# Kernel optimization log

Hardware: AMD Instinct MI355X
Metric: run time of the kernel (lower is better)

## Reference

```python
import jax, jax.numpy as jnp
import numpy as np

NUM_USERS = 100000
NUM_ITEMS = 50000
EMB_DIM = 64
N_LAYERS = 3
NUM_BICLIQUES = 20000
E_ADJ = 1200000
E_HV = 400000
E_HU = 400000


def setup_inputs() -> dict:
    key = jax.random.key(0)
    ks = jax.random.split(key, 11)
    N = NUM_USERS + NUM_ITEMS
    return {
        "user_emb": jax.random.normal(ks[0], (NUM_USERS, EMB_DIM), dtype=jnp.float32) * 0.1,
        "item_emb": jax.random.normal(ks[1], (NUM_ITEMS, EMB_DIM), dtype=jnp.float32) * 0.1,
        "adj_val": jax.random.uniform(ks[2], (E_ADJ,), dtype=jnp.float32),
        "hv_val": jax.random.uniform(ks[3], (E_HV,), dtype=jnp.float32),
        "hu_val": jax.random.uniform(ks[4], (E_HU,), dtype=jnp.float32),
        "adj_row": jax.random.randint(ks[5], (E_ADJ,), 0, N, dtype=jnp.int32),
        "adj_col": jax.random.randint(ks[6], (E_ADJ,), 0, N, dtype=jnp.int32),
        "hv_row": jax.random.randint(ks[7], (E_HV,), 0, NUM_BICLIQUES, dtype=jnp.int32),
        "hv_col": jax.random.randint(ks[8], (E_HV,), 0, NUM_ITEMS, dtype=jnp.int32),
        "hu_row": jax.random.randint(ks[9], (E_HU,), 0, NUM_USERS, dtype=jnp.int32),
        "hu_col": jax.random.randint(ks[10], (E_HU,), 0, NUM_BICLIQUES, dtype=jnp.int32),
    }


def _spmm(row, col, val, x, n_rows):
    # sparse [n_rows, n_cols] @ dense [n_cols, d] via gather + segment-sum
    return jax.ops.segment_sum(val[:, None] * x[col], row, num_segments=n_rows)


def _row_degree(row, val, n_rows):
    deg = jax.ops.segment_sum(val, row, num_segments=n_rows)
    return jnp.where(deg == 0, 1.0, deg)  # matches degree[degree == 0] = 1.0


def reference(user_emb, item_emb, adj_val, hv_val, hu_val,
              adj_row, adj_col, hv_row, hv_col, hu_row, hu_col):
    N = user_emb.shape[0] + item_emb.shape[0]
    # ---- LightGCN global encoder: mean over layer embeddings ----
    all_emb = jnp.concatenate([user_emb, item_emb], axis=0)  # [N, d]
    acc = all_emb
    e = all_emb
    for _ in range(N_LAYERS):
        e = _spmm(adj_row, adj_col, adj_val, e, N)
        acc = acc + e
    final = acc / (N_LAYERS + 1)
    u_global = final[: user_emb.shape[0]]
    i_global = final[user_emb.shape[0]:]
    # ---- Biclique local encoder ----
    biclique_feat = _spmm(hv_row, hv_col, hv_val, item_emb, NUM_BICLIQUES)  # [B, d]
    biclique_feat = biclique_feat / _row_degree(hv_row, hv_val, NUM_BICLIQUES)[:, None]
    u_local = _spmm(hu_row, hu_col, hu_val, biclique_feat, user_emb.shape[0])  # [U, d]
    u_local = u_local / _row_degree(hu_row, hu_val, user_emb.shape[0])[:, None]
    return (u_global + u_local, i_global)
```

## Files before the change

kernel.cpp:

```cpp
#include <hip/hip_runtime.h>

#define NUSERS 100000
#define NITEMS 50000
#define NTOT   150000
#define NBIC   20000
#define DIM    64

#define HV_BASE  NTOT
#define HU_BASE  (NTOT + NBIC)
#define NROWS_ALL (NTOT + NBIC + NUSERS)

#define ADJ_RPB  500
#define NB_ADJ   300
#define HV_RPB   200
#define NB_HV    100
#define HU_RPB   1000
#define NB_HU    100
#define NBKT     (NB_ADJ + NB_HV + NB_HU)
#define HSIZE    512

#define EDGE_CAP 5120
#define ROWS_CAP 1024
#define CHUNK    8192
#define PA_BLK   1024
#define PB_BLK   512

typedef _Float16 h8 __attribute__((ext_vector_type(8)));

__device__ __forceinline__ void bucket_of(int r, int& b, int& rl) {
    if (r < NTOT)          { int q = r / ADJ_RPB;               b = q;                rl = r - q * ADJ_RPB; }
    else if (r < HU_BASE)  { int rr = r - HV_BASE; int q = rr / HV_RPB;
                             b = NB_ADJ + q;                    rl = rr - q * HV_RPB; }
    else                   { int rr = r - HU_BASE; int q = rr / HU_RPB;
                             b = NB_ADJ + NB_HV + q;            rl = rr - q * HU_RPB; }
}

__global__ void to_half_kernel(const float* __restrict__ user,
                               const float* __restrict__ item,
                               _Float16* __restrict__ x16) {
    int i = blockIdx.x * blockDim.x + threadIdx.x;
    const int n8 = NTOT * DIM / 8;
    if (i >= n8) return;
    const int u8 = NUSERS * DIM / 8;
    const float4* src = (i < u8) ? (const float4*)user + 2 * (size_t)i
                                 : (const float4*)item + 2 * (size_t)(i - u8);
    float4 a = src[0], b = src[1];
    h8 h;
    h[0] = (_Float16)a.x; h[1] = (_Float16)a.y; h[2] = (_Float16)a.z; h[3] = (_Float16)a.w;
    h[4] = (_Float16)b.x; h[5] = (_Float16)b.y; h[6] = (_Float16)b.z; h[7] = (_Float16)b.w;
    ((h8*)x16)[i] = h;
}

__global__ void __launch_bounds__(PA_BLK)
phaseA_kernel(const int* __restrict__ adj_row, const int* __restrict__ adj_col,
              const float* __restrict__ adj_val,
              const int* __restrict__ hv_row, const int* __restrict__ hv_col,
              const float* __restrict__ hv_val,
              const int* __restrict__ hu_row, const int* __restrict__ hu_col,
              const float* __restrict__ hu_val,
              int* __restrict__ bkt_cnt, int2* __restrict__ tmp,
              int e_adj, int e_hv, int e_hu) {
    __shared__ int hist[HSIZE];
    __shared__ int lstart[HSIZE];
    __shared__ int destB[HSIZE];
    __shared__ int psum[HSIZE];
    __shared__ int2 stage[CHUNK];

    const int tid = threadIdx.x;
    const int e_all = e_adj + e_hv + e_hu;
    const int base = blockIdx.x * CHUNK;
    const int nloc = min(CHUNK, e_all - base);

    if (tid < HSIZE) hist[tid] = 0;
    __syncthreads();

    for (int i = tid; i < nloc; i += PA_BLK) {
        int t = base + i, r;
        if (t < e_adj)             r = adj_row[t];
        else if (t < e_adj + e_hv) r = HV_BASE + hv_row[t - e_adj];
        else                       r = HU_BASE + hu_row[t - e_adj - e_hv];
        int b, rl; bucket_of(r, b, rl);
        atomicAdd(&hist[b], 1);
    }
    __syncthreads();

    int v = 0;
    if (tid < HSIZE) { v = hist[tid]; psum[tid] = v; }
    __syncthreads();
    for (int off = 1; off < HSIZE; off <<= 1) {
        int t = 0;
        if (tid < HSIZE && tid >= off) t = psum[tid - off];
        __syncthreads();
        if (tid < HSIZE) psum[tid] += t;
        __syncthreads();
    }
    if (tid < HSIZE) lstart[tid] = psum[tid] - v;
    __syncthreads();

    if (tid < NBKT) {
        int c = hist[tid];
        if (c > 0)
            destB[tid] = tid * EDGE_CAP + atomicAdd(&bkt_cnt[tid], c) - lstart[tid];
    }
    __syncthreads();
    if (tid < HSIZE) hist[tid] = lstart[tid];
    __syncthreads();

    for (int i = tid; i < nloc; i += PA_BLK) {
        int t = base + i, r, c; float v2;
        if (t < e_adj)             { r = adj_row[t]; c = adj_col[t]; v2 = adj_val[t]; }
        else if (t < e_adj + e_hv) { int k = t - e_adj;
                                     r = HV_BASE + hv_row[k]; c = hv_col[k]; v2 = hv_val[k]; }
        else                       { int k = t - e_adj - e_hv;
                                     r = HU_BASE + hu_row[k]; c = hu_col[k]; v2 = hu_val[k]; }
        int b, rl; bucket_of(r, b, rl);
        int p = atomicAdd(&hist[b], 1);
        stage[p] = make_int2(c | (rl << 18), __float_as_int(v2));
    }
    __syncthreads();

    const int wave = tid >> 6, lane = tid & 63;
    for (int b = wave; b < NBKT; b += (PA_BLK / 64)) {
        int s = lstart[b];
        int e = hist[b];
        int d = destB[b];
        for (int j = s + lane; j < e; j += 64)
            tmp[d + j] = stage[j];
    }
}

__global__ void bkt_scan(const int* __restrict__ cnt, int* __restrict__ base) {
    __shared__ int s[HSIZE];
    int tid = threadIdx.x;
    int v = (tid < NBKT) ? cnt[tid] : 0;
    s[tid] = v;
    __syncthreads();
    for (int off = 1; off < HSIZE; off <<= 1) {
        int t = (tid >= off) ? s[tid - off] : 0;
        __syncthreads();
        s[tid] += t;
        __syncthreads();
    }
    if (tid < NBKT) base[tid] = s[tid] - v;
}

__global__ void __launch_bounds__(PB_BLK)
phaseB_kernel(const int* __restrict__ bkt_cnt, const int* __restrict__ bkt_base,
              const int2* __restrict__ tmp, int2* __restrict__ edges,
              int* __restrict__ start, int* __restrict__ cntArr) {
    __shared__ int  rh[ROWS_CAP];
    __shared__ int  rs[ROWS_CAP];
    __shared__ int  psum[PB_BLK];
    __shared__ int2 stage[EDGE_CAP];

    const int tid = threadIdx.x;
    const int b = blockIdx.x;
    int rlo, nR;
    if (b < NB_ADJ)              { rlo = b * ADJ_RPB;                          nR = ADJ_RPB; }
    else if (b < NB_ADJ + NB_HV) { rlo = HV_BASE + (b - NB_ADJ) * HV_RPB;      nR = HV_RPB; }
    else                         { rlo = HU_BASE + (b - NB_ADJ - NB_HV) * HU_RPB; nR = HU_RPB; }

    const int nE = bkt_cnt[b];
    const int gbase = bkt_base[b];
    const int2* src = tmp + (size_t)b * EDGE_CAP;

    rh[tid] = 0;
    rh[tid + PB_BLK] = 0;
    __syncthreads();

    for (int i = tid; i < nE; i += PB_BLK) {
        int2 e = src[i];
        atomicAdd(&rh[((unsigned)e.x) >> 18], 1);
    }
    __syncthreads();

    int a0 = rh[2 * tid], a1 = rh[2 * tid + 1];
    int tot = a0 + a1;
    psum[tid] = tot;
    __syncthreads();
    for (int off = 1; off < PB_BLK; off <<= 1) {
        int v = (tid >= off) ? psum[tid - off] : 0;
        __syncthreads();
        psum[tid] += v;
        __syncthreads();
    }
    int ex = psum[tid] - tot;
    rs[2 * tid]     = ex;
    rs[2 * tid + 1] = ex + a0;
    __syncthreads();

    for (int i = tid; i < nR; i += PB_BLK) {
        start[rlo + i]  = gbase + rs[i];
        cntArr[rlo + i] = rh[i];
    }
    __syncthreads();

    for (int i = tid; i < nE; i += PB_BLK) {
        int2 e = src[i];
        int rl = ((unsigned)e.x) >> 18;
        int p = atomicAdd(&rs[rl], 1);
        stage[p] = make_int2(e.x & 0x3FFFF, e.y);
    }
    __syncthreads();
    for (int i = tid; i < nE; i += PB_BLK) edges[gbase + i] = stage[i];
}

__global__ void gather_h(const int* __restrict__ start, const int* __restrict__ cnt,
                         const int2* __restrict__ edges,
                         const _Float16* __restrict__ x, _Float16* __restrict__ out,
                         int nrows) {
    int gid = blockIdx.x * (blockDim.x >> 3) + (threadIdx.x >> 3);
    if (gid >= nrows) return;
    int c = (threadIdx.x & 7) << 3;
    int s = start[gid], n = cnt[gid];
    float acc[8] = {0.f, 0.f, 0.f, 0.f, 0.f, 0.f, 0.f, 0.f};
    for (int j = s; j < s + n; ++j) {
        int2 e = edges[j];
        float v = __int_as_float(e.y);
        h8 xv = *(const h8*)(x + (size_t)e.x * DIM + c);
        #pragma unroll
        for (int k = 0; k < 8; ++k) acc[k] += v * (float)xv[k];
    }
    h8 o;
    #pragma unroll
    for (int k = 0; k < 8; ++k) o[k] = (_Float16)acc[k];
    *(h8*)(out + (size_t)gid * DIM + c) = o;
}

__global__ void gather_norm_h(const int* __restrict__ start, const int* __restrict__ cnt,
                              const int2* __restrict__ edges,
                              const _Float16* __restrict__ x, _Float16* __restrict__ out,
                              int nrows) {
    int gid = blockIdx.x * (blockDim.x >> 3) + (threadIdx.x >> 3);
    if (gid >= nrows) return;
    int c = (threadIdx.x & 7) << 3;
    int s = start[gid], n = cnt[gid];
    float acc[8] = {0.f, 0.f, 0.f, 0.f, 0.f, 0.f, 0.f, 0.f};
    float deg = 0.f;
    for (int j = s; j < s + n; ++j) {
        int2 e = edges[j];
        float v = __int_as_float(e.y);
        deg += v;
        h8 xv = *(const h8*)(x + (size_t)e.x * DIM + c);
        #pragma unroll
        for (int k = 0; k < 8; ++k) acc[k] += v * (float)xv[k];
    }
    if (deg == 0.f) deg = 1.f;
    float inv = 1.f / deg;
    h8 o;
    #pragma unroll
    for (int k = 0; k < 8; ++k) o[k] = (_Float16)(acc[k] * inv);
    *(h8*)(out + (size_t)gid * DIM + c) = o;
}

__global__ void gather_final_h(const int* __restrict__ start, const int* __restrict__ cnt,
                               const int2* __restrict__ edges,
                               const _Float16* __restrict__ X16,
                               const _Float16* __restrict__ T0,
                               const _Float16* __restrict__ T1,
                               const _Float16* __restrict__ ulocal,
                               float* __restrict__ out) {
    int gid = blockIdx.x * (blockDim.x >> 3) + (threadIdx.x >> 3);
    if (gid >= NTOT) return;
    int c = (threadIdx.x & 7) << 3;
    int s = start[gid], n = cnt[gid];
    float acc[8] = {0.f, 0.f, 0.f, 0.f, 0.f, 0.f, 0.f, 0.f};
    for (int j = s; j < s + n; ++j) {
        int2 e = edges[j];
        float v = __int_as_float(e.y);
        h8 xv = *(const h8*)(T1 + (size_t)e.x * DIM + c);
        #pragma unroll
        for (int k = 0; k < 8; ++k) acc[k] += v * (float)xv[k];
    }
    size_t o = (size_t)gid * DIM + c;
    h8 x0 = *(const h8*)(X16 + o);
    h8 t0 = *(const h8*)(T0 + o);
    h8 t1 = *(const h8*)(T1 + o);
    float r[8];
    #pragma unroll
    for (int k = 0; k < 8; ++k)
        r[k] = 0.25f * ((float)x0[k] + (float)t0[k] + (float)t1[k] + acc[k]);
    if (gid < NUSERS) {
        h8 ul = *(const h8*)(ulocal + o);
        #pragma unroll
        for (int k = 0; k < 8; ++k) r[k] += (float)ul[k];
    }
    float4 lo = make_float4(r[0], r[1], r[2], r[3]);
    float4 hi = make_float4(r[4], r[5], r[6], r[7]);
    float4* op = (float4*)(out + o);
    op[0] = lo;
    op[1] = hi;
}

extern "C" void kernel_launch(void* const* d_in, const int* in_sizes, int n_in,
                              void* d_out, int out_size, void* d_ws, size_t ws_size,
                              hipStream_t stream) {
    const float* user_emb = (const float*)d_in[0];
    const float* item_emb = (const float*)d_in[1];
    const float* adj_val  = (const float*)d_in[2];
    const float* hv_val   = (const float*)d_in[3];
    const float* hu_val   = (const float*)d_in[4];
    const int*   adj_row  = (const int*)d_in[5];
    const int*   adj_col  = (const int*)d_in[6];
    const int*   hv_row   = (const int*)d_in[7];
    const int*   hv_col   = (const int*)d_in[8];
    const int*   hu_row   = (const int*)d_in[9];
    const int*   hu_col   = (const int*)d_in[10];

    const int E_ADJ = in_sizes[2];
    const int E_HV  = in_sizes[3];
    const int E_HU  = in_sizes[4];
    const int E_ALL = E_ADJ + E_HV + E_HU;

    char* ws = (char*)d_ws;
    auto alloc = [&](size_t bytes) -> char* {
        char* p = ws;
        ws += (bytes + 255) & ~(size_t)255;
        return p;
    };
    const size_t SZ_H = (size_t)NTOT * DIM * sizeof(_Float16);
    _Float16* X16     = (_Float16*)alloc(SZ_H);
    _Float16* T0      = (_Float16*)alloc(SZ_H);
    _Float16* T1      = (_Float16*)alloc(SZ_H);
    _Float16* bic     = (_Float16*)alloc((size_t)NBIC * DIM * sizeof(_Float16));
    _Float16* ulocal  = (_Float16*)alloc((size_t)NUSERS * DIM * sizeof(_Float16));
    int*   cnt      = (int*)alloc((size_t)NROWS_ALL * sizeof(int));
    int*   start    = (int*)alloc((size_t)NROWS_ALL * sizeof(int));
    int2*  edges    = (int2*)alloc((size_t)E_ALL * sizeof(int2));
    int2*  tmp      = (int2*)alloc((size_t)NBKT * EDGE_CAP * sizeof(int2));
    int*   bkt_cnt  = (int*)alloc(NBKT * sizeof(int));
    int*   bkt_base = (int*)alloc(NBKT * sizeof(int));

    const int BLK = 256;
    auto cdiv = [](int a, int b) { return (a + b - 1) / b; };

    hipMemsetAsync(bkt_cnt, 0, NBKT * sizeof(int), stream);
    phaseA_kernel<<<cdiv(E_ALL, CHUNK), PA_BLK, 0, stream>>>(adj_row, adj_col, adj_val,
                                                             hv_row, hv_col, hv_val,
                                                             hu_row, hu_col, hu_val,
                                                             bkt_cnt, tmp, E_ADJ, E_HV, E_HU);
    to_half_kernel<<<cdiv(NTOT * DIM / 8, BLK), BLK, 0, stream>>>(user_emb, item_emb, X16);
    bkt_scan<<<1, HSIZE, 0, stream>>>(bkt_cnt, bkt_base);
    phaseB_kernel<<<NBKT, PB_BLK, 0, stream>>>(bkt_cnt, bkt_base, tmp, edges, start, cnt);

    const int RPB = BLK >> 3;

    gather_h<<<cdiv(NTOT, RPB), BLK, 0, stream>>>(start, cnt, edges, X16, T0, NTOT);
    gather_h<<<cdiv(NTOT, RPB), BLK, 0, stream>>>(start, cnt, edges, T0, T1, NTOT);
    gather_norm_h<<<cdiv(NBIC, RPB), BLK, 0, stream>>>(start + HV_BASE, cnt + HV_BASE, edges,
                                                       X16 + (size_t)NUSERS * DIM, bic, NBIC);
    gather_norm_h<<<cdiv(NUSERS, RPB), BLK, 0, stream>>>(start + HU_BASE, cnt + HU_BASE, edges,
                                                         bic, ulocal, NUSERS);
    gather_final_h<<<cdiv(NTOT, RPB), BLK, 0, stream>>>(start, cnt, edges,
                                                        X16, T0, T1, ulocal, (float*)d_out);
}
```

Baseline: 301.7 us.

## Degree-sort rows per bucket and fuse independent gather launches

```diff
diff --git a/kernel.cpp b/kernel.cpp
--- a/kernel.cpp
+++ b/kernel.cpp
@@ -21,6 +21,7 @@
 
 #define EDGE_CAP 5120
 #define ROWS_CAP 1024
+#define NCLS     64
 #define CHUNK    8192
 #define PA_BLK   1024
 #define PB_BLK   512
@@ -147,10 +148,13 @@
 __global__ void __launch_bounds__(PB_BLK)
 phaseB_kernel(const int* __restrict__ bkt_cnt, const int* __restrict__ bkt_base,
               const int2* __restrict__ tmp, int2* __restrict__ edges,
-              int* __restrict__ start, int* __restrict__ cntArr) {
+              int* __restrict__ start, int* __restrict__ cntArr,
+              int* __restrict__ perm) {
     __shared__ int  rh[ROWS_CAP];
     __shared__ int  rs[ROWS_CAP];
     __shared__ int  psum[PB_BLK];
+    __shared__ int  clsh[NCLS];
+    __shared__ int  clsb[NCLS];
     __shared__ int2 stage[EDGE_CAP];
 
     const int tid = threadIdx.x;
@@ -166,6 +170,7 @@
 
     rh[tid] = 0;
     rh[tid + PB_BLK] = 0;
+    if (tid < NCLS) clsh[tid] = 0;
     __syncthreads();
 
     for (int i = tid; i < nE; i += PB_BLK) {
@@ -192,6 +197,26 @@
     for (int i = tid; i < nR; i += PB_BLK) {
         start[rlo + i]  = gbase + rs[i];
         cntArr[rlo + i] = rh[i];
+        atomicAdd(&clsh[min(rh[i], NCLS - 1)], 1);
+    }
+    __syncthreads();
+
+    if (tid < NCLS) clsb[tid] = clsh[tid];
+    __syncthreads();
+    for (int off = 1; off < NCLS; off <<= 1) {
+        int v = 0;
+        if (tid < NCLS && tid >= off) v = clsb[tid - off];
+        __syncthreads();
+        if (tid < NCLS) clsb[tid] += v;
+        __syncthreads();
+    }
+    if (tid < NCLS) clsb[tid] -= clsh[tid];
+    __syncthreads();
+
+    for (int i = tid; i < nR; i += PB_BLK) {
+        int cls = min(rh[i], NCLS - 1);
+        int pos = atomicAdd(&clsb[cls], 1);
+        perm[rlo + pos] = rlo + i;
     }
     __syncthreads();
 
@@ -205,88 +230,128 @@
     for (int i = tid; i < nE; i += PB_BLK) edges[gbase + i] = stage[i];
 }
 
-__global__ void gather_h(const int* __restrict__ start, const int* __restrict__ cnt,
-                         const int2* __restrict__ edges,
-                         const _Float16* __restrict__ x, _Float16* __restrict__ out,
-                         int nrows) {
-    int gid = blockIdx.x * (blockDim.x >> 3) + (threadIdx.x >> 3);
-    if (gid >= nrows) return;
+__device__ __forceinline__ void gather_row(const int2* __restrict__ edges,
+                                           const _Float16* __restrict__ x,
+                                           int s, int n, int c, float* acc) {
+    float acc1[8] = {0.f, 0.f, 0.f, 0.f, 0.f, 0.f, 0.f, 0.f};
+    int j = s, e = s + n;
+    for (; j + 1 < e; j += 2) {
+        int2 e0 = edges[j], e1 = edges[j + 1];
+        float v0 = __int_as_float(e0.y), v1 = __int_as_float(e1.y);
+        h8 x0 = *(const h8*)(x + (size_t)e0.x * DIM + c);
+        h8 x1 = *(const h8*)(x + (size_t)e1.x * DIM + c);
+        #pragma unroll
+        for (int k = 0; k < 8; ++k) { acc[k] += v0 * (float)x0[k]; acc1[k] += v1 * (float)x1[k]; }
+    }
+    if (j < e) {
+        int2 e0 = edges[j];
+        float v0 = __int_as_float(e0.y);
+        h8 x0 = *(const h8*)(x + (size_t)e0.x * DIM + c);
+        #pragma unroll
+        for (int k = 0; k < 8; ++k) acc[k] += v0 * (float)x0[k];
+    }
+    #pragma unroll
+    for (int k = 0; k < 8; ++k) acc[k] += acc1[k];
+}
+
+__global__ void gatherK1(const int* __restrict__ start, const int* __restrict__ cnt,
+                         const int2* __restrict__ edges, const int* __restrict__ perm,
+                         const _Float16* __restrict__ X16,
+                         _Float16* __restrict__ T0, _Float16* __restrict__ bic,
+                         int gA) {
     int c = (threadIdx.x & 7) << 3;
-    int s = start[gid], n = cnt[gid];
-    float acc[8] = {0.f, 0.f, 0.f, 0.f, 0.f, 0.f, 0.f, 0.f};
-    for (int j = s; j < s + n; ++j) {
-        int2 e = edges[j];
-        float v = __int_as_float(e.y);
-        h8 xv = *(const h8*)(x + (size_t)e.x * DIM + c);
-        #pragma unroll
-        for (int k = 0; k < 8; ++k) acc[k] += v * (float)xv[k];
-    }
-    h8 o;
-    #pragma unroll
-    for (int k = 0; k < 8; ++k) o[k] = (_Float16)acc[k];
-    *(h8*)(out + (size_t)gid * DIM + c) = o;
-}
-
-__global__ void gather_norm_h(const int* __restrict__ start, const int* __restrict__ cnt,
-                              const int2* __restrict__ edges,
-                              const _Float16* __restrict__ x, _Float16* __restrict__ out,
-                              int nrows) {
-    int gid = blockIdx.x * (blockDim.x >> 3) + (threadIdx.x >> 3);
-    if (gid >= nrows) return;
+    int lrow = threadIdx.x >> 3;
+    if (blockIdx.x < gA) {
+        int gid = blockIdx.x * 32 + lrow;
+        if (gid >= NTOT) return;
+        int r = perm[gid];
+        float acc[8] = {0.f, 0.f, 0.f, 0.f, 0.f, 0.f, 0.f, 0.f};
+        gather_row(edges, X16, start[r], cnt[r], c, acc);
+        h8 o;
+        #pragma unroll
+        for (int k = 0; k < 8; ++k) o[k] = (_Float16)acc[k];
+        *(h8*)(T0 + (size_t)r * DIM + c) = o;
+    } else {
+        int gid = (blockIdx.x - gA) * 32 + lrow;
+        if (gid >= NBIC) return;
+        int r = perm[HV_BASE + gid];
+        int s = start[r], n = cnt[r];
+        float acc[8] = {0.f, 0.f, 0.f, 0.f, 0.f, 0.f, 0.f, 0.f};
+        gather_row(edges, X16 + (size_t)NUSERS * DIM, s, n, c, acc);
+        float deg = 0.f;
+        for (int j = s; j < s + n; ++j) deg += __int_as_float(edges[j].y);
+        if (deg == 0.f) deg = 1.f;
+        float inv = 1.f / deg;
+        h8 o;
+        #pragma unroll
+        for (int k = 0; k < 8; ++k) o[k] = (_Float16)(acc[k] * inv);
+        *(h8*)(bic + (size_t)(r - HV_BASE) * DIM + c) = o;
+    }
+}
+
+__global__ void gatherK2(const int* __restrict__ start, const int* __restrict__ cnt,
+                         const int2* __restrict__ edges, const int* __restrict__ perm,
+                         const _Float16* __restrict__ T0, const _Float16* __restrict__ bic,
+                         _Float16* __restrict__ T1, _Float16* __restrict__ ulocal,
+                         int gA) {
     int c = (threadIdx.x & 7) << 3;
-    int s = start[gid], n = cnt[gid];
-    float acc[8] = {0.f, 0.f, 0.f, 0.f, 0.f, 0.f, 0.f, 0.f};
-    float deg = 0.f;
-    for (int j = s; j < s + n; ++j) {
-        int2 e = edges[j];
-        float v = __int_as_float(e.y);
-        deg += v;
-        h8 xv = *(const h8*)(x + (size_t)e.x * DIM + c);
-        #pragma unroll
-        for (int k = 0; k < 8; ++k) acc[k] += v * (float)xv[k];
-    }
-    if (deg == 0.f) deg = 1.f;
-    float inv = 1.f / deg;
-    h8 o;
-    #pragma unroll
-    for (int k = 0; k < 8; ++k) o[k] = (_Float16)(acc[k] * inv);
-    *(h8*)(out + (size_t)gid * DIM + c) = o;
-}
-
-__global__ void gather_final_h(const int* __restrict__ start, const int* __restrict__ cnt,
-                               const int2* __restrict__ edges,
-                               const _Float16* __restrict__ X16,
-                               const _Float16* __restrict__ T0,
-                               const _Float16* __restrict__ T1,
-                               const _Float16* __restrict__ ulocal,
-                               float* __restrict__ out) {
-    int gid = blockIdx.x * (blockDim.x >> 3) + (threadIdx.x >> 3);
+    int lrow = threadIdx.x >> 3;
+    if (blockIdx.x < gA) {
+        int gid = blockIdx.x * 32 + lrow;
+        if (gid >= NTOT) return;
+        int r = perm[gid];
+        float acc[8] = {0.f, 0.f, 0.f, 0.f, 0.f, 0.f, 0.f, 0.f};
+        gather_row(edges, T0, start[r], cnt[r], c, acc);
+        h8 o;
+        #pragma unroll
+        for (int k = 0; k < 8; ++k) o[k] = (_Float16)acc[k];
+        *(h8*)(T1 + (size_t)r * DIM + c) = o;
+    } else {
+        int gid = (blockIdx.x - gA) * 32 + lrow;
+        if (gid >= NUSERS) return;
+        int r = perm[HU_BASE + gid];
+        int s = start[r], n = cnt[r];
+        float acc[8] = {0.f, 0.f, 0.f, 0.f, 0.f, 0.f, 0.f, 0.f};
+        gather_row(edges, bic, s, n, c, acc);
+        float deg = 0.f;
+        for (int j = s; j < s + n; ++j) deg += __int_as_float(edges[j].y);
+        if (deg == 0.f) deg = 1.f;
+        float inv = 1.f / deg;
+        h8 o;
+        #pragma unroll
+        for (int k = 0; k < 8; ++k) o[k] = (_Float16)(acc[k] * inv);
+        *(h8*)(ulocal + (size_t)(r - HU_BASE) * DIM + c) = o;
+    }
+}
+
+__global__ void gatherK3(const int* __restrict__ start, const int* __restrict__ cnt,
+                         const int2* __restrict__ edges, const int* __restrict__ perm,
+                         const _Float16* __restrict__ X16,
+                         const _Float16* __restrict__ T0,
+                         const _Float16* __restrict__ T1,
+                         const _Float16* __restrict__ ulocal,
+                         float* __restrict__ out) {
+    int gid = blockIdx.x * 32 + (threadIdx.x >> 3);
     if (gid >= NTOT) return;
     int c = (threadIdx.x & 7) << 3;
-    int s = start[gid], n = cnt[gid];
+    int r = perm[gid];
     float acc[8] = {0.f, 0.f, 0.f, 0.f, 0.f, 0.f, 0.f, 0.f};
-    for (int j = s; j < s + n; ++j) {
-        int2 e = edges[j];
-        float v = __int_as_float(e.y);
-        h8 xv = *(const h8*)(T1 + (size_t)e.x * DIM + c);
-        #pragma unroll
-        for (int k = 0; k < 8; ++k) acc[k] += v * (float)xv[k];
-    }
-    size_t o = (size_t)gid * DIM + c;
+    gather_row(edges, T1, start[r], cnt[r], c, acc);
+    size_t o = (size_t)r * DIM + c;
     h8 x0 = *(const h8*)(X16 + o);
     h8 t0 = *(const h8*)(T0 + o);
     h8 t1 = *(const h8*)(T1 + o);
-    float r[8];
+    float rr[8];
     #pragma unroll
     for (int k = 0; k < 8; ++k)
-        r[k] = 0.25f * ((float)x0[k] + (float)t0[k] + (float)t1[k] + acc[k]);
-    if (gid < NUSERS) {
+        rr[k] = 0.25f * ((float)x0[k] + (float)t0[k] + (float)t1[k] + acc[k]);
+    if (r < NUSERS) {
         h8 ul = *(const h8*)(ulocal + o);
         #pragma unroll
-        for (int k = 0; k < 8; ++k) r[k] += (float)ul[k];
-    }
-    float4 lo = make_float4(r[0], r[1], r[2], r[3]);
-    float4 hi = make_float4(r[4], r[5], r[6], r[7]);
+        for (int k = 0; k < 8; ++k) rr[k] += (float)ul[k];
+    }
+    float4 lo = make_float4(rr[0], rr[1], rr[2], rr[3]);
+    float4 hi = make_float4(rr[4], rr[5], rr[6], rr[7]);
     float4* op = (float4*)(out + o);
     op[0] = lo;
     op[1] = hi;
@@ -326,6 +391,7 @@
     _Float16* ulocal  = (_Float16*)alloc((size_t)NUSERS * DIM * sizeof(_Float16));
     int*   cnt      = (int*)alloc((size_t)NROWS_ALL * sizeof(int));
     int*   start    = (int*)alloc((size_t)NROWS_ALL * sizeof(int));
+    int*   perm     = (int*)alloc((size_t)NROWS_ALL * sizeof(int));
     int2*  edges    = (int2*)alloc((size_t)E_ALL * sizeof(int2));
     int2*  tmp      = (int2*)alloc((size_t)NBKT * EDGE_CAP * sizeof(int2));
     int*   bkt_cnt  = (int*)alloc(NBKT * sizeof(int));
@@ -341,16 +407,15 @@
                                                              bkt_cnt, tmp, E_ADJ, E_HV, E_HU);
     to_half_kernel<<<cdiv(NTOT * DIM / 8, BLK), BLK, 0, stream>>>(user_emb, item_emb, X16);
     bkt_scan<<<1, HSIZE, 0, stream>>>(bkt_cnt, bkt_base);
-    phaseB_kernel<<<NBKT, PB_BLK, 0, stream>>>(bkt_cnt, bkt_base, tmp, edges, start, cnt);
-
-    const int RPB = BLK >> 3;
-
-    gather_h<<<cdiv(NTOT, RPB), BLK, 0, stream>>>(start, cnt, edges, X16, T0, NTOT);
-    gather_h<<<cdiv(NTOT, RPB), BLK, 0, stream>>>(start, cnt, edges, T0, T1, NTOT);
-    gather_norm_h<<<cdiv(NBIC, RPB), BLK, 0, stream>>>(start + HV_BASE, cnt + HV_BASE, edges,
-                                                       X16 + (size_t)NUSERS * DIM, bic, NBIC);
-    gather_norm_h<<<cdiv(NUSERS, RPB), BLK, 0, stream>>>(start + HU_BASE, cnt + HU_BASE, edges,
-                                                         bic, ulocal, NUSERS);
-    gather_final_h<<<cdiv(NTOT, RPB), BLK, 0, stream>>>(start, cnt, edges,
-                                                        X16, T0, T1, ulocal, (float*)d_out);
-}
+    phaseB_kernel<<<NBKT, PB_BLK, 0, stream>>>(bkt_cnt, bkt_base, tmp, edges,
+                                               start, cnt, perm);
+
+    const int gA  = cdiv(NTOT, 32);
+    const int gHV = cdiv(NBIC, 32);
+    const int gHU = cdiv(NUSERS, 32);
+
+    gatherK1<<<gA + gHV, BLK, 0, stream>>>(start, cnt, edges, perm, X16, T0, bic, gA);
+    gatherK2<<<gA + gHU, BLK, 0, stream>>>(start, cnt, edges, perm, T0, bic, T1, ulocal, gA);
+    gatherK3<<<gA, BLK, 0, stream>>>(start, cnt, edges, perm, X16, T0, T1, ulocal,
+                                     (float*)d_out);
+}
```

After: 276.2 us. 8.5% less time.
